# Optimization experiments

Hardware: AMD Instinct MI355X
Metric: run time of the kernel (lower is better)

Reference implementation:

```python
import jax, jax.numpy as jnp
import numpy as np

L, E, H, R = 6, 1024, 8, 33
DH = E // H
FF = 4 * E
B, S = 8, 512


def _layer_norm(x, g, b, eps=1e-5):
    m = jnp.mean(x, axis=-1, keepdims=True)
    v = jnp.mean(jnp.square(x - m), axis=-1, keepdims=True)
    return (x - m) * jax.lax.rsqrt(v + eps) * g + b


def setup_inputs() -> dict:
    key = jax.random.key(0)
    ks = jax.random.split(key, 24)
    rn = lambda k, shape, s=0.02: (jax.random.normal(k, shape, jnp.float32) * s)
    inp = {
        'enc_padded': jax.random.normal(ks[0], (B, S, E), jnp.float32),
        'relations': jax.random.randint(ks[1], (B, S, S), 0, R),
        'enc_lengths': jax.random.randint(ks[2], (B,), 1, S + 1),
        'Wq': rn(ks[3], (L, E, E)), 'bq': jnp.zeros((L, E), jnp.float32),
        'Wk': rn(ks[4], (L, E, E)), 'bk': jnp.zeros((L, E), jnp.float32),
        'Wv': rn(ks[5], (L, E, E)), 'bv': jnp.zeros((L, E), jnp.float32),
        'Wo': rn(ks[6], (L, E, E)), 'bo': jnp.zeros((L, E), jnp.float32),
        'rel_k': rn(ks[7], (L, R, DH)),
        'rel_v': rn(ks[8], (L, R, DH)),
        'W1': rn(ks[9], (L, E, FF)), 'b1': jnp.zeros((L, FF), jnp.float32),
        'W2': rn(ks[10], (L, FF, E)), 'b2': jnp.zeros((L, E), jnp.float32),
        'ln1_g': jnp.ones((L, E), jnp.float32), 'ln1_b': jnp.zeros((L, E), jnp.float32),
        'ln2_g': jnp.ones((L, E), jnp.float32), 'ln2_b': jnp.zeros((L, E), jnp.float32),
        'lnf_g': jnp.ones((E,), jnp.float32), 'lnf_b': jnp.zeros((E,), jnp.float32),
    }
    return inp


def reference(enc_padded, relations, enc_lengths, Wq, bq, Wk, bk, Wv, bv, Wo, bo,
              rel_k, rel_v, W1, b1, W2, b2, ln1_g, ln1_b, ln2_g, ln2_b, lnf_g, lnf_b):
    x = enc_padded  # [B,S,E]
    dt = x.dtype
    # attention mask: valid iff both query and key positions are within seq length
    pos = jnp.arange(S)
    valid = pos[None, :] < enc_lengths[:, None]            # [B,S]
    mask2d = valid[:, :, None] & valid[:, None, :]          # [B,S,S]
    # one-hot relation indicator, shared across layers (R=33 is small)
    rel_oh = jax.nn.one_hot(relations, R, dtype=dt)        # [B,S,S,R]
    scale = 1.0 / np.sqrt(DH).astype(np.float32)

    def split_heads(t):  # [B,S,E] -> [B,H,S,DH]
        return t.reshape(B, S, H, DH).transpose(0, 2, 1, 3)

    for l in range(L):
        # --- relation-aware self-attention (pre-LN sublayer) ---
        h = _layer_norm(x, ln1_g[l], ln1_b[l])
        q = split_heads(h @ Wq[l] + bq[l])
        k = split_heads(h @ Wk[l] + bk[l])
        v = split_heads(h @ Wv[l] + bv[l])
        scores = jnp.einsum('bhid,bhjd->bhij', q, k)
        # relation key bias: q_i . rel_k[rel[i,j]]  via small [B,H,S,R] GEMM + one-hot contraction
        qr = jnp.einsum('bhid,rd->bhir', q, rel_k[l])
        scores = (scores + jnp.einsum('bhir,bijr->bhij', qr, rel_oh)) * scale
        scores = jnp.where(mask2d[:, None], scores, jnp.asarray(-1e9, dt))
        attn = jax.nn.softmax(scores, axis=-1)              # [B,H,S,S]
        out = jnp.einsum('bhij,bhjd->bhid', attn, v)
        # relation value bias: sum_j attn_ij * rel_v[rel[i,j]]
        a_rel = jnp.einsum('bhij,bijr->bhir', attn, rel_oh)
        out = out + jnp.einsum('bhir,rd->bhid', a_rel, rel_v[l])
        out = out.transpose(0, 2, 1, 3).reshape(B, S, E) @ Wo[l] + bo[l]
        x = x + out
        # --- position-wise feed-forward (pre-LN sublayer) ---
        h2 = _layer_norm(x, ln2_g[l], ln2_b[l])
        x = x + (jax.nn.relu(h2 @ W1[l] + b1[l]) @ W2[l] + b2[l])
    return _layer_norm(x, lnf_g, lnf_b)
```

## Files before the change

kernel.cpp:

```cpp
#include <hip/hip_runtime.h>

#define LNUM 6
#define EDIM 1024
#define HNUM 8
#define DHD  128
#define RNUM 33
#define FFD  4096
#define BNUM 8
#define SLEN 512
#define TOK  (BNUM*SLEN)

typedef __attribute__((ext_vector_type(8))) short bf16x8;
typedef __attribute__((ext_vector_type(4))) float f32x4;
typedef unsigned short u16;
typedef unsigned int u32;

__device__ __forceinline__ u16 f2b(float f) {
  u32 u = __builtin_bit_cast(u32, f);
  u32 r = u + 0x7FFFu + ((u >> 16) & 1u);
  return (u16)(r >> 16);
}
__device__ __forceinline__ u32 pck(float a, float b) { return (u32)f2b(a) | ((u32)f2b(b) << 16); }

#define GL16(gp, lp) __builtin_amdgcn_global_load_lds(                        \
    (const __attribute__((address_space(1))) void*)(gp),                      \
    (__attribute__((address_space(3))) void*)(lp), 16, 0, 0)

template<int BF16OUT>
__global__ __launch_bounds__(256) void ln_kernel(const float* __restrict__ x,
                                                 const float* __restrict__ g,
                                                 const float* __restrict__ be,
                                                 void* __restrict__ o) {
  int row = blockIdx.x;
  int t = threadIdx.x;
  const float* xr = x + (size_t)row * EDIM;
  float4 xv = *reinterpret_cast<const float4*>(xr + t * 4);
  float s1 = xv.x + xv.y + xv.z + xv.w;
  float s2 = xv.x*xv.x + xv.y*xv.y + xv.z*xv.z + xv.w*xv.w;
#pragma unroll
  for (int off = 32; off >= 1; off >>= 1) {
    s1 += __shfl_down(s1, off, 64);
    s2 += __shfl_down(s2, off, 64);
  }
  __shared__ float r1[4], r2[4];
  if ((t & 63) == 0) { r1[t >> 6] = s1; r2[t >> 6] = s2; }
  __syncthreads();
  s1 = r1[0] + r1[1] + r1[2] + r1[3];
  s2 = r2[0] + r2[1] + r2[2] + r2[3];
  float mean = s1 * (1.0f / EDIM);
  float var  = s2 * (1.0f / EDIM) - mean * mean;
  float rstd = rsqrtf(var + 1e-5f);
  float4 gv = *reinterpret_cast<const float4*>(g + t * 4);
  float4 bv = *reinterpret_cast<const float4*>(be + t * 4);
  float o0 = (xv.x - mean) * rstd * gv.x + bv.x;
  float o1 = (xv.y - mean) * rstd * gv.y + bv.y;
  float o2 = (xv.z - mean) * rstd * gv.z + bv.z;
  float o3 = (xv.w - mean) * rstd * gv.w + bv.w;
  if (BF16OUT) {
    ushort4 ov; ov.x = f2b(o0); ov.y = f2b(o1); ov.z = f2b(o2); ov.w = f2b(o3);
    *reinterpret_cast<ushort4*>((u16*)o + (size_t)row * EDIM + t * 4) = ov;
  } else {
    *reinterpret_cast<float4*>((float*)o + (size_t)row * EDIM + t * 4) = make_float4(o0, o1, o2, o3);
  }
}

__global__ __launch_bounds__(256) void wtrans(const float* __restrict__ src0,
                                              u16* __restrict__ dst0,
                                              int Kd, int Nd, size_t sstride, size_t dstride) {
  __shared__ float Ts[32][33];
  const float* src = src0 + blockIdx.z * sstride;
  u16* dst = dst0 + blockIdx.z * dstride;
  int r0 = blockIdx.y * 32, c0 = blockIdx.x * 32;
  int ty = threadIdx.x >> 3, tx = threadIdx.x & 7;
  float4 v = *reinterpret_cast<const float4*>(src + (size_t)(r0 + ty) * Nd + c0 + tx * 4);
  Ts[ty][tx*4+0] = v.x; Ts[ty][tx*4+1] = v.y; Ts[ty][tx*4+2] = v.z; Ts[ty][tx*4+3] = v.w;
  __syncthreads();
  ushort4 o;
  o.x = f2b(Ts[tx*4+0][ty]); o.y = f2b(Ts[tx*4+1][ty]);
  o.z = f2b(Ts[tx*4+2][ty]); o.w = f2b(Ts[tx*4+3][ty]);
  *reinterpret_cast<ushort4*>(dst + (size_t)(c0 + ty) * Kd + r0 + tx * 4) = o;
}

__global__ __launch_bounds__(256) void relpack(const int* __restrict__ rel,
                                               unsigned char* __restrict__ out) {
  __shared__ int Ts[32][33];
  int bz = blockIdx.z;
  int r0 = blockIdx.y * 32, c0 = blockIdx.x * 32;
  int ty = threadIdx.x >> 3, tx = threadIdx.x & 7;
  const int* src = rel + (size_t)bz * SLEN * SLEN;
  int4 v = *reinterpret_cast<const int4*>(src + (size_t)(r0 + ty) * SLEN + c0 + tx * 4);
  Ts[ty][tx*4+0] = v.x; Ts[ty][tx*4+1] = v.y; Ts[ty][tx*4+2] = v.z; Ts[ty][tx*4+3] = v.w;
  __syncthreads();
  u32 o = (u32)(Ts[tx*4+0][ty] & 255) | ((u32)(Ts[tx*4+1][ty] & 255) << 8) |
          ((u32)(Ts[tx*4+2][ty] & 255) << 16) | ((u32)(Ts[tx*4+3][ty] & 255) << 24);
  *reinterpret_cast<u32*>(out + (size_t)bz * SLEN * SLEN + (size_t)(c0 + ty) * SLEN + r0 + tx * 4) = o;
}

template<int BIASMODE, int ACT, int RES, int OUTBF16>
__global__ __launch_bounds__(256) void gemm_bt(const u16* __restrict__ A,
                                               const u16* __restrict__ B,
                                               const float* __restrict__ bias0,
                                               const float* __restrict__ bias1,
                                               const float* __restrict__ res,
                                               void* __restrict__ Cv,
                                               int M, int N, int K) {
  __shared__ u16 As[128 * 64];
  __shared__ u16 Bs[128 * 64];
  int t = threadIdx.x;
  int l = t & 63, w = t >> 6;
  int wm = w & 1, wn = w >> 1;
  int nwg = gridDim.x * gridDim.y;
  int bid = blockIdx.y * gridDim.x + blockIdx.x;
  int cpx = nwg >> 3;
  int swz = (bid & 7) * cpx + (bid >> 3);
  int m0 = (swz / gridDim.x) * 128, n0 = (swz % gridDim.x) * 128;
  f32x4 acc[4][4] = {};
  const u16* Agp = A + (size_t)(m0 + w * 32 + (l >> 3)) * K + (l & 7) * 8;
  const u16* Bgp = B + (size_t)(n0 + w * 32 + (l >> 3)) * K + (l & 7) * 8;
  u16* Alp = As + w * 4 * 512;
  u16* Blp = Bs + w * 4 * 512;
  for (int k0 = 0; k0 < K; k0 += 64) {
    __syncthreads();
#pragma unroll
    for (int u = 0; u < 4; ++u) {
      GL16(Agp + (size_t)(u * 8) * K + k0, Alp + u * 512);
      GL16(Bgp + (size_t)(u * 8) * K + k0, Blp + u * 512);
    }
    __syncthreads();
#pragma unroll
    for (int d4 = 0; d4 < 2; ++d4) {
      bf16x8 af[4];
#pragma unroll
      for (int fm = 0; fm < 4; ++fm) {
        int row = wm * 64 + fm * 16 + (l & 15);
        af[fm] = *reinterpret_cast<const bf16x8*>(As + row * 64 + (d4 * 4 + (l >> 4)) * 8);
      }
#pragma unroll
      for (int fn = 0; fn < 4; ++fn) {
        int row = wn * 64 + fn * 16 + (l & 15);
        bf16x8 bf = *reinterpret_cast<const bf16x8*>(Bs + row * 64 + (d4 * 4 + (l >> 4)) * 8);
#pragma unroll
        for (int fm = 0; fm < 4; ++fm)
          acc[fm][fn] = __builtin_amdgcn_mfma_f32_16x16x32_bf16(af[fm], bf, acc[fm][fn], 0, 0, 0);
      }
    }
  }
#pragma unroll
  for (int fm = 0; fm < 4; ++fm)
#pragma unroll
    for (int fn = 0; fn < 4; ++fn)
#pragma unroll
      for (int e = 0; e < 4; ++e) {
        int m = m0 + wm * 64 + fm * 16 + (l >> 4) * 4 + e;
        int n = n0 + wn * 64 + fn * 16 + (l & 15);
        float v = acc[fm][fn][e];
        if (BIASMODE == 0) v += bias0[n];
        if (BIASMODE == 1) v += bias0[m];
        if (BIASMODE == 2) v += (n < 1024) ? bias0[n] : bias1[n - 1024];
        if (ACT == 1) v = fmaxf(v, 0.f);
        if (RES == 1) v += res[(size_t)m * N + n];
        if (OUTBF16) ((u16*)Cv)[(size_t)m * N + n] = f2b(v);
        else ((float*)Cv)[(size_t)m * N + n] = v;
      }
}

#define A_P  0
#define A_Q  16384
#define A_PS 32768
#define A_QR 40960
#define A_AR 50176
#define A_LS 59392
#define A_SM 59648

#define WAITVM4 do { asm volatile("s_waitcnt vmcnt(4)" ::: "memory"); \
                     __builtin_amdgcn_sched_barrier(0); } while (0)
#define WAITVM0 do { asm volatile("s_waitcnt vmcnt(0)" ::: "memory"); \
                     __builtin_amdgcn_sched_barrier(0); } while (0)

__global__ __launch_bounds__(256, 2) void attn_kernel(const u16* __restrict__ qk,
                                                      const u16* __restrict__ vt,
                                                      const unsigned char* __restrict__ rel8,
                                                      const int* __restrict__ lens,
                                                      const float* __restrict__ relk,
                                                      const float* __restrict__ relv,
                                                      u16* __restrict__ outb) {
  __align__(16) __shared__ char sm[A_SM];
  char*  Pb  = sm + A_P;
  char*  Qb  = sm + A_Q;
  char*  PSb = sm + A_PS;
  float* QR  = (float*)(sm + A_QR);
  float* AREL = (float*)(sm + A_AR);
  float* LSUM = (float*)(sm + A_LS);

  const int t = threadIdx.x;
  const int l = t & 63, w = t >> 6;
  const int lg = l >> 4;
  const int ll = l & 15;
  const int bx = blockIdx.x;
  const int xcd = bx & 7, rem = bx >> 3, slot = rem & 7, it = rem >> 3;
  const int g = slot * 8 + xcd;
  const int b = g >> 3, hh = g & 7;
  const int i0 = it * 64;
  const int len = lens[b];
  const float scale = 0.08838834764831845f;
  char* PSw = PSb + w * 2048;

  auto issueK = [&](int kt) {
#pragma unroll
    for (int u = 0; u < 4; ++u) {
      int row = w * 16 + u * 4 + (lg);
      int sb = (ll * 16) ^ (((u * 4 + lg) & 7) << 4);
      const u16* gp = qk + (size_t)(b * SLEN + kt * 64 + row) * 2048 + 1024 + hh * DHD + (sb >> 1);
      GL16(gp, Pb + (w * 4 + u) * 1024);
    }
  };
  auto issueV = [&](int kt) {
#pragma unroll
    for (int u = 0; u < 4; ++u) {
      int row = w * 32 + u * 8 + (l >> 3);
      int sb = ((l & 7) * 16) ^ ((l >> 3) << 4);
      const u16* gp = vt + (size_t)(hh * DHD + row) * TOK + b * SLEN + kt * 64 + (sb >> 1);
      GL16(gp, Qb + (w * 4 + u) * 1024);
    }
  };

  u32 relw[4];
  const unsigned char* relbase = rel8 + (size_t)b * SLEN * SLEN + (i0 + w * 16 + lg * 4);
  {
    const unsigned char* rb = relbase + (size_t)ll * SLEN;
#pragma unroll
    for (int fj = 0; fj < 4; ++fj)
      relw[fj] = *reinterpret_cast<const u32*>(rb + (size_t)(fj * 16) * SLEN);
  }
  for (int idx = l; idx < 16 * 36; idx += 64) AREL[w * 16 * 36 + idx] = 0.f;
  if (t < 192) {
    int r = t >> 2, sub = t & 3;
#pragma unroll
    for (int u = 0; u < 4; ++u) {
      int seg = sub * 4 + u;
      uint4 o;
      if (r < RNUM) {
        float4 f0 = *reinterpret_cast<const float4*>(relk + r * DHD + seg * 8);
        float4 f1 = *reinterpret_cast<const float4*>(relk + r * DHD + seg * 8 + 4);
        o.x = pck(f0.x, f0.y); o.y = pck(f0.z, f0.w);
        o.z = pck(f1.x, f1.y); o.w = pck(f1.z, f1.w);
      } else { o.x = o.y = o.z = o.w = 0u; }
      *reinterpret_cast<uint4*>(Pb + r * 256 + ((seg * 16) ^ ((r & 7) << 4))) = o;
    }
  }
  bf16x8 aq[4];
  {
    const u16* qrow = qk + (size_t)(b * SLEN + i0 + w * 16 + ll) * 2048 + hh * DHD;
#pragma unroll
    for (int d4 = 0; d4 < 4; ++d4)
      aq[d4] = *reinterpret_cast<const bf16x8*>(qrow + (d4 * 4 + lg) * 8);
  }
  __syncthreads();
#pragma unroll
  for (int rb = 0; rb < 3; ++rb) {
    f32x4 acc = {};
#pragma unroll
    for (int d4 = 0; d4 < 4; ++d4) {
      int rr = rb * 16 + ll;
      bf16x8 br = *reinterpret_cast<const bf16x8*>(Pb + rr * 256 + (((d4 * 4 + lg) * 16) ^ ((rr & 7) << 4)));
      acc = __builtin_amdgcn_mfma_f32_16x16x32_bf16(aq[d4], br, acc, 0, 0, 0);
    }
    int col = rb * 16 + ll;
    if (col < 36)
#pragma unroll
      for (int e = 0; e < 4; ++e)
        QR[(w * 16 + lg * 4 + e) * 36 + col] = acc[e];
  }
  __syncthreads();
  issueK(0);

  bool rowv[4];
#pragma unroll
  for (int e = 0; e < 4; ++e) rowv[e] = (i0 + w * 16 + lg * 4 + e) < len;

  float m_[4];
#pragma unroll
  for (int e = 0; e < 4; ++e) m_[e] = -3.0e38f;
  f32x4 oacc[8] = {};

  for (int kt = 0; kt < 8; ++kt) {
    issueV(kt);
    WAITVM4;
    __builtin_amdgcn_s_barrier();
    __builtin_amdgcn_s_setprio(1);
    f32x4 sacc[4];
#pragma unroll
    for (int fj = 0; fj < 4; ++fj) {
      f32x4 a = {};
#pragma unroll
      for (int d4 = 0; d4 < 4; ++d4) {
        int row = fj * 16 + ll;
        bf16x8 bk_ = *reinterpret_cast<const bf16x8*>(Pb + row * 256 + (((d4 * 4 + lg) * 16) ^ ((row & 7) << 4)));
        a = __builtin_amdgcn_mfma_f32_16x16x32_bf16(aq[d4], bk_, a, 0, 0, 0);
      }
      sacc[fj] = a;
    }
    __builtin_amdgcn_s_setprio(0);
#pragma unroll
    for (int fj = 0; fj < 4; ++fj) {
      bool colv = (kt * 64 + fj * 16 + ll) < len;
      u32 rw = relw[fj];
#pragma unroll
      for (int e = 0; e < 4; ++e) {
        int r = (rw >> (8 * e)) & 255;
        float s = (sacc[fj][e] + QR[(w * 16 + lg * 4 + e) * 36 + r]) * scale;
        s = (rowv[e] && colv) ? s : -1e9f;
        sacc[fj][e] = s;
      }
    }
    float pl[4];
#pragma unroll
    for (int e = 0; e < 4; ++e)
      pl[e] = fmaxf(fmaxf(sacc[0][e], sacc[1][e]), fmaxf(sacc[2][e], sacc[3][e]));
    bool ok = (pl[0] <= m_[0] + 8.f) && (pl[1] <= m_[1] + 8.f) &&
              (pl[2] <= m_[2] + 8.f) && (pl[3] <= m_[3] + 8.f);
    if (!__all(ok)) {
#pragma unroll
      for (int e = 0; e < 4; ++e) {
        float px = pl[e];
        px = fmaxf(px, __shfl_xor(px, 1, 64));
        px = fmaxf(px, __shfl_xor(px, 2, 64));
        px = fmaxf(px, __shfl_xor(px, 4, 64));
        px = fmaxf(px, __shfl_xor(px, 8, 64));
        float mn = fmaxf(m_[e], px);
        float f = __expf(m_[e] - mn);
        m_[e] = mn;
#pragma unroll
        for (int fd = 0; fd < 8; ++fd) oacc[fd][e] *= f;
        if (f != 1.0f) {
          int row = w * 16 + lg * 4 + e;
          AREL[row * 36 + ll] *= f;
          AREL[row * 36 + 16 + ll] *= f;
          if (ll == 0) AREL[row * 36 + 32] *= f;
        }
      }
    }
#pragma unroll
    for (int fj = 0; fj < 4; ++fj) {
      u32 rw = relw[fj];
#pragma unroll
      for (int e = 0; e < 4; ++e) {
        float p = __expf(sacc[fj][e] - m_[e]);
        int iloc = lg * 4 + e;
        atomicAdd(&AREL[(w * 16 + iloc) * 36 + ((rw >> (8 * e)) & 255)], p);
        *reinterpret_cast<u16*>(PSw + iloc * 128 + (((fj * 16 + ll) * 2) ^ ((iloc & 7) << 4))) = f2b(p);
      }
    }
    if (kt < 7) {
      const unsigned char* rb = relbase + (size_t)((kt + 1) * 64 + ll) * SLEN;
#pragma unroll
      for (int fj = 0; fj < 4; ++fj)
        relw[fj] = *reinterpret_cast<const u32*>(rb + (size_t)(fj * 16) * SLEN);
    }
    __builtin_amdgcn_s_barrier();
    if (kt < 7) issueK(kt + 1);
    if (kt < 7) { WAITVM4; } else { WAITVM0; }
    __builtin_amdgcn_s_barrier();
    __builtin_amdgcn_s_setprio(1);
#pragma unroll
    for (int kc = 0; kc < 2; ++kc) {
      bf16x8 pa = *reinterpret_cast<const bf16x8*>(PSw + ll * 128 + (((kc * 4 + lg) * 16) ^ ((ll & 7) << 4)));
#pragma unroll
      for (int fd = 0; fd < 8; ++fd) {
        int row = fd * 16 + ll;
        bf16x8 vb = *reinterpret_cast<const bf16x8*>(Qb + row * 128 + (((kc * 4 + lg) * 16) ^ ((row & 7) << 4)));
        oacc[fd] = __builtin_amdgcn_mfma_f32_16x16x32_bf16(pa, vb, oacc[fd], 0, 0, 0);
      }
    }
    __builtin_amdgcn_s_setprio(0);
    __builtin_amdgcn_s_barrier();
  }
  if (l < 16) {
    int row = w * 16 + l;
    float s = 0.f;
    for (int r = 0; r < RNUM; ++r) s += AREL[row * 36 + r];
    LSUM[row] = s;
  }
#pragma unroll
  for (int e = 0; e < 4; ++e) {
    float inv = 1.0f / LSUM[w * 16 + lg * 4 + e];
#pragma unroll
    for (int fd = 0; fd < 8; ++fd) oacc[fd][e] *= inv;
  }
  for (int idx = t; idx < 128 * 64; idx += 256) {
    int d = idx >> 6, r = idx & 63;
    u16 v = (r < RNUM) ? f2b(relv[r * DHD + d]) : (u16)0;
    *reinterpret_cast<u16*>(Pb + d * 128 + ((r * 2) ^ ((d & 7) << 4))) = v;
  }
  for (int idx = l; idx < 1024; idx += 64) {
    int ri = idx >> 6, r = idx & 63;
    int row = w * 16 + ri;
    float v = (r < RNUM) ? AREL[row * 36 + r] * (1.0f / LSUM[row]) : 0.f;
    *reinterpret_cast<u16*>(PSw + ri * 128 + ((r * 2) ^ ((ri & 7) << 4))) = f2b(v);
  }
  __syncthreads();
#pragma unroll
  for (int kc = 0; kc < 2; ++kc) {
    bf16x8 pa = *reinterpret_cast<const bf16x8*>(PSw + ll * 128 + (((kc * 4 + lg) * 16) ^ ((ll & 7) << 4)));
#pragma unroll
    for (int fd = 0; fd < 8; ++fd) {
      int row = fd * 16 + ll;
      bf16x8 vb = *reinterpret_cast<const bf16x8*>(Pb + row * 128 + (((kc * 4 + lg) * 16) ^ ((row & 7) << 4)));
      oacc[fd] = __builtin_amdgcn_mfma_f32_16x16x32_bf16(pa, vb, oacc[fd], 0, 0, 0);
    }
  }
  char* OSw = Qb + w * 4096;
#pragma unroll
  for (int fd = 0; fd < 8; ++fd)
#pragma unroll
    for (int e = 0; e < 4; ++e)
      *reinterpret_cast<u16*>(OSw + ((lg * 4 + e) * 128 + fd * 16 + ll) * 2) = f2b(oacc[fd][e]);
  __syncthreads();
  {
    int ri = l >> 2, q4 = l & 3;
    const char* srcb = OSw + ri * 256 + q4 * 64;
    u16* dst = outb + (size_t)(b * SLEN + i0 + w * 16 + ri) * EDIM + hh * DHD + q4 * 32;
    uint4 x0 = *reinterpret_cast<const uint4*>(srcb);
    uint4 x1 = *reinterpret_cast<const uint4*>(srcb + 16);
    uint4 x2 = *reinterpret_cast<const uint4*>(srcb + 32);
    uint4 x3 = *reinterpret_cast<const uint4*>(srcb + 48);
    *reinterpret_cast<uint4*>(dst)      = x0;
    *reinterpret_cast<uint4*>(dst + 8)  = x1;
    *reinterpret_cast<uint4*>(dst + 16) = x2;
    *reinterpret_cast<uint4*>(dst + 24) = x3;
  }
}

extern "C" void kernel_launch(void* const* d_in, const int* in_sizes, int n_in,
                              void* d_out, int out_size, void* d_ws, size_t ws_size,
                              hipStream_t stream) {
  const float* enc  = (const float*)d_in[0];
  const int*   rel  = (const int*)d_in[1];
  const int*   lens = (const int*)d_in[2];
  const float* Wq = (const float*)d_in[3];
  const float* bq = (const float*)d_in[4];
  const float* Wk = (const float*)d_in[5];
  const float* bk = (const float*)d_in[6];
  const float* Wv = (const float*)d_in[7];
  const float* bv = (const float*)d_in[8];
  const float* Wo = (const float*)d_in[9];
  const float* bo = (const float*)d_in[10];
  const float* relk = (const float*)d_in[11];
  const float* relv = (const float*)d_in[12];
  const float* W1 = (const float*)d_in[13];
  const float* b1 = (const float*)d_in[14];
  const float* W2 = (const float*)d_in[15];
  const float* b2 = (const float*)d_in[16];
  const float* ln1g = (const float*)d_in[17];
  const float* ln1b = (const float*)d_in[18];
  const float* ln2g = (const float*)d_in[19];
  const float* ln2b = (const float*)d_in[20];
  const float* lnfg = (const float*)d_in[21];
  const float* lnfb = (const float*)d_in[22];
  float* out = (float*)d_out;

  char* W = (char*)d_ws;
  u16* h     = (u16*)W;
  unsigned char* rel8 = (unsigned char*)W;
  char* U    = W + 8388608;
  u16* qkb   = (u16*)U;
  u16* vtb   = (u16*)(U + 16777216);
  u16* attno = (u16*)(U + 25165824);
  u16* mid   = (u16*)U;
  bool xin = ws_size >= (size_t)83886080;
  float* x = xin ? (float*)(W + 41943040) : out;
  char* WT = W + (xin ? 58720256 : 41943040);
  bool big = ws_size >= (size_t)209715200;

  const size_t EE = (size_t)EDIM * EDIM;
  const size_t EF = (size_t)EDIM * FFD;

  u16 *WqkT, *WvT, *WoT, *W1T, *W2T;
  dim3 blk(256);
  if (big) {
    u16* wqk_all = (u16*)WT;
    u16* wv_all  = wqk_all + 6 * 2 * EE;
    u16* wo_all  = wv_all + 6 * EE;
    u16* w1_all  = wo_all + 6 * EE;
    u16* w2_all  = w1_all + 6 * EF;
    wtrans<<<dim3(32, 32, 6), blk, 0, stream>>>(Wq, wqk_all, 1024, 1024, EE, 2 * EE);
    wtrans<<<dim3(32, 32, 6), blk, 0, stream>>>(Wk, wqk_all + EE, 1024, 1024, EE, 2 * EE);
    wtrans<<<dim3(32, 32, 6), blk, 0, stream>>>(Wv, wv_all, 1024, 1024, EE, EE);
    wtrans<<<dim3(32, 32, 6), blk, 0, stream>>>(Wo, wo_all, 1024, 1024, EE, EE);
    wtrans<<<dim3(128, 32, 6), blk, 0, stream>>>(W1, w1_all, 1024, 4096, EF, EF);
    wtrans<<<dim3(32, 128, 6), blk, 0, stream>>>(W2, w2_all, 4096, 1024, EF, EF);
    WqkT = wqk_all; WvT = wv_all; WoT = wo_all; W1T = w1_all; W2T = w2_all;
  } else {
    WqkT = (u16*)WT;
    WvT  = WqkT + 2 * EE;
    WoT  = WvT + EE;
    W1T  = WoT + EE;
    W2T  = W1T + EF;
  }

  dim3 gLN(TOK);
  for (int ll = 0; ll < LNUM; ++ll) {
    u16 *wqkT, *wvT, *woT, *w1T, *w2T;
    if (big) {
      wqkT = WqkT + (size_t)ll * 2 * EE; wvT = WvT + (size_t)ll * EE; woT = WoT + (size_t)ll * EE;
      w1T = W1T + (size_t)ll * EF; w2T = W2T + (size_t)ll * EF;
    } else {
      wqkT = WqkT; wvT = WvT; woT = WoT; w1T = W1T; w2T = W2T;
      wtrans<<<dim3(32, 32, 1), blk, 0, stream>>>(Wq + ll * EE, wqkT, 1024, 1024, 0, 0);
      wtrans<<<dim3(32, 32, 1), blk, 0, stream>>>(Wk + ll * EE, wqkT + EE, 1024, 1024, 0, 0);
      wtrans<<<dim3(32, 32, 1), blk, 0, stream>>>(Wv + ll * EE, wvT, 1024, 1024, 0, 0);
      wtrans<<<dim3(32, 32, 1), blk, 0, stream>>>(Wo + ll * EE, woT, 1024, 1024, 0, 0);
      wtrans<<<dim3(128, 32, 1), blk, 0, stream>>>(W1 + ll * EF, w1T, 1024, 4096, 0, 0);
      wtrans<<<dim3(32, 128, 1), blk, 0, stream>>>(W2 + ll * EF, w2T, 4096, 1024, 0, 0);
    }
    const float* xin_p = (ll == 0) ? enc : x;
    ln_kernel<1><<<gLN, blk, 0, stream>>>(xin_p, ln1g + ll * EDIM, ln1b + ll * EDIM, h);
    gemm_bt<2, 0, 0, 1><<<dim3(16, 32), blk, 0, stream>>>(h, wqkT, bq + ll * EDIM, bk + ll * EDIM,
                                                          nullptr, qkb, TOK, 2048, EDIM);
    gemm_bt<1, 0, 0, 1><<<dim3(32, 8), blk, 0, stream>>>(wvT, h, bv + ll * EDIM, nullptr,
                                                         nullptr, vtb, EDIM, TOK, EDIM);
    relpack<<<dim3(16, 16, 8), blk, 0, stream>>>(rel, rel8);
    attn_kernel<<<dim3(512), blk, 0, stream>>>(qkb, vtb, rel8, lens,
                                               relk + (size_t)ll * RNUM * DHD,
                                               relv + (size_t)ll * RNUM * DHD, attno);
    gemm_bt<0, 0, 1, 0><<<dim3(8, 32), blk, 0, stream>>>(attno, woT, bo + ll * EDIM, nullptr,
                                                         xin_p, x, TOK, EDIM, EDIM);
    ln_kernel<1><<<gLN, blk, 0, stream>>>(x, ln2g + ll * EDIM, ln2b + ll * EDIM, h);
    gemm_bt<0, 1, 0, 1><<<dim3(32, 32), blk, 0, stream>>>(h, w1T, b1 + ll * FFD, nullptr,
                                                          nullptr, mid, TOK, FFD, EDIM);
    gemm_bt<0, 0, 1, 0><<<dim3(8, 32), blk, 0, stream>>>(mid, w2T, b2 + ll * EDIM, nullptr,
                                                         x, x, TOK, EDIM, FFD);
  }
  ln_kernel<0><<<gLN, blk, 0, stream>>>(x, lnfg, lnfb, out);
}
```

Baseline: 2.297 ms.

## Double-buffer GEMM LDS tiles with async prefetch of next K-slice

After: 2.207 ms. -3.9%, faster.

```diff
diff --git a/kernel.cpp b/kernel.cpp
--- a/kernel.cpp
+++ b/kernel.cpp
@@ -25,6 +25,13 @@
 #define GL16(gp, lp) __builtin_amdgcn_global_load_lds(                        \
     (const __attribute__((address_space(1))) void*)(gp),                      \
     (__attribute__((address_space(3))) void*)(lp), 16, 0, 0)
+
+#define WAITVM8 do { asm volatile("s_waitcnt vmcnt(8)" ::: "memory"); \
+                     __builtin_amdgcn_sched_barrier(0); } while (0)
+#define WAITVM4 do { asm volatile("s_waitcnt vmcnt(4)" ::: "memory"); \
+                     __builtin_amdgcn_sched_barrier(0); } while (0)
+#define WAITVM0 do { asm volatile("s_waitcnt vmcnt(0)" ::: "memory"); \
+                     __builtin_amdgcn_sched_barrier(0); } while (0)
 
 template<int BF16OUT>
 __global__ __launch_bounds__(256) void ln_kernel(const float* __restrict__ x,
@@ -104,46 +111,49 @@
                                                const float* __restrict__ res,
                                                void* __restrict__ Cv,
                                                int M, int N, int K) {
-  __shared__ u16 As[128 * 64];
-  __shared__ u16 Bs[128 * 64];
+  __shared__ u16 As[2][128 * 64];
+  __shared__ u16 Bs[2][128 * 64];
   int t = threadIdx.x;
   int l = t & 63, w = t >> 6;
   int wm = w & 1, wn = w >> 1;
-  int nwg = gridDim.x * gridDim.y;
-  int bid = blockIdx.y * gridDim.x + blockIdx.x;
-  int cpx = nwg >> 3;
-  int swz = (bid & 7) * cpx + (bid >> 3);
-  int m0 = (swz / gridDim.x) * 128, n0 = (swz % gridDim.x) * 128;
+  int m0 = blockIdx.y * 128, n0 = blockIdx.x * 128;
   f32x4 acc[4][4] = {};
   const u16* Agp = A + (size_t)(m0 + w * 32 + (l >> 3)) * K + (l & 7) * 8;
   const u16* Bgp = B + (size_t)(n0 + w * 32 + (l >> 3)) * K + (l & 7) * 8;
-  u16* Alp = As + w * 4 * 512;
-  u16* Blp = Bs + w * 4 * 512;
-  for (int k0 = 0; k0 < K; k0 += 64) {
-    __syncthreads();
+  const int nst = K >> 6;
+  auto issue = [&](int k0, int bi) {
 #pragma unroll
     for (int u = 0; u < 4; ++u) {
-      GL16(Agp + (size_t)(u * 8) * K + k0, Alp + u * 512);
-      GL16(Bgp + (size_t)(u * 8) * K + k0, Blp + u * 512);
-    }
-    __syncthreads();
+      GL16(Agp + (size_t)(u * 8) * K + k0, &As[bi][w * 2048 + u * 512]);
+      GL16(Bgp + (size_t)(u * 8) * K + k0, &Bs[bi][w * 2048 + u * 512]);
+    }
+  };
+  issue(0, 0);
+  for (int i = 0; i < nst; ++i) {
+    int cur = i & 1;
+    if (i + 1 < nst) { issue((i + 1) * 64, cur ^ 1); WAITVM8; }
+    else             { WAITVM0; }
+    __builtin_amdgcn_s_barrier();
+    const u16* Asc = As[cur];
+    const u16* Bsc = Bs[cur];
 #pragma unroll
     for (int d4 = 0; d4 < 2; ++d4) {
       bf16x8 af[4];
 #pragma unroll
       for (int fm = 0; fm < 4; ++fm) {
         int row = wm * 64 + fm * 16 + (l & 15);
-        af[fm] = *reinterpret_cast<const bf16x8*>(As + row * 64 + (d4 * 4 + (l >> 4)) * 8);
+        af[fm] = *reinterpret_cast<const bf16x8*>(Asc + row * 64 + (d4 * 4 + (l >> 4)) * 8);
       }
 #pragma unroll
       for (int fn = 0; fn < 4; ++fn) {
         int row = wn * 64 + fn * 16 + (l & 15);
-        bf16x8 bf = *reinterpret_cast<const bf16x8*>(Bs + row * 64 + (d4 * 4 + (l >> 4)) * 8);
+        bf16x8 bf = *reinterpret_cast<const bf16x8*>(Bsc + row * 64 + (d4 * 4 + (l >> 4)) * 8);
 #pragma unroll
         for (int fm = 0; fm < 4; ++fm)
           acc[fm][fn] = __builtin_amdgcn_mfma_f32_16x16x32_bf16(af[fm], bf, acc[fm][fn], 0, 0, 0);
       }
     }
+    __builtin_amdgcn_s_barrier();
   }
 #pragma unroll
   for (int fm = 0; fm < 4; ++fm)
@@ -171,11 +181,6 @@
 #define A_AR 50176
 #define A_LS 59392
 #define A_SM 59648
-
-#define WAITVM4 do { asm volatile("s_waitcnt vmcnt(4)" ::: "memory"); \
-                     __builtin_amdgcn_sched_barrier(0); } while (0)
-#define WAITVM0 do { asm volatile("s_waitcnt vmcnt(0)" ::: "memory"); \
-                     __builtin_amdgcn_sched_barrier(0); } while (0)
 
 __global__ __launch_bounds__(256, 2) void attn_kernel(const u16* __restrict__ qk,
                                                       const u16* __restrict__ vt,
```
